# Performance work log

Hardware: AMD Instinct MI355X
Metric: run time of the kernel (lower is better)

The kernel has to match this reference:

```python
import jax, jax.numpy as jnp
import numpy as np

N_NODES = 100000
N_EDGES = 600000
D_FEAT = 128
D_DOT = 4


def setup_inputs() -> dict:
    key = jax.random.key(0)
    k1, k2, k3, k4, k5 = jax.random.split(key, 5)
    n = jax.random.normal(k1, (N_NODES, D_FEAT), dtype=jnp.float32)
    e = jax.random.normal(k2, (N_EDGES, D_FEAT), dtype=jnp.float32)
    # xavier_uniform for Linear(D_FEAT, D_DOT); bias filled with 0
    limit = float(np.sqrt(6.0 / (D_FEAT + D_DOT)))
    W = jax.random.uniform(k3, (D_DOT, D_FEAT), dtype=jnp.float32, minval=-limit, maxval=limit)
    b = jnp.zeros((D_DOT,), dtype=jnp.float32)
    src_idx = jax.random.randint(k4, (N_EDGES,), 0, N_NODES, dtype=jnp.int64)
    dst_idx = jax.random.randint(k5, (N_EDGES,), 0, N_NODES, dtype=jnp.int64)
    return {"n": n, "e": e, "W": W, "b": b, "src_idx": src_idx, "dst_idx": dst_idx}


def reference(n, e, W, b, src_idx, dst_idx):
    # gather per-edge src/dst node features: [E, D]
    src = n[src_idx]
    dst = n[dst_idx]
    # include_edge_features=True: mean of node and edge features
    src = (src + e) * 0.5
    dst = (dst + e) * 0.5
    # tiny linear projection to dot_product_dim=4: [E, 4]
    hs = src @ W.T + b
    hd = dst @ W.T + b
    # per-edge dot product (bmm of [E,1,4] x [E,4,1] -> [E,1]) then sigmoid
    score = jax.nn.sigmoid(jnp.sum(hs * hd, axis=-1, keepdims=True))
    return score
```

## Files before the change

### kernel.cpp

```cpp
#include <hip/hip_runtime.h>
#include <math.h>

#define D_FEAT 128
#define D_DOT  4


__device__ __forceinline__ float dot4(const float4 a, const float4 b) {
    return a.x * b.x + a.y * b.y + a.z * b.z + a.w * b.w;
}

__global__ __launch_bounds__(256, 6) void node_proj_kernel(
    const float* __restrict__ n,
    const float* __restrict__ W,
    float* __restrict__ pn,
    int n_nodes)
{
    const int t    = threadIdx.x;
    const int lane = t & 63;
    const int sub  = lane & 15;
    const int g    = lane >> 4;
    const int wave = t >> 6;
    const int base = blockIdx.x * 32 + wave * 8;
    const int last = n_nodes - 1;

    const float4* W4 = reinterpret_cast<const float4*>(W);
    float4 wlo[D_DOT], whi[D_DOT];
#pragma unroll
    for (int k = 0; k < D_DOT; ++k) {
        wlo[k] = W4[k * 32 + sub];
        whi[k] = W4[k * 32 + sub + 16];
    }

    const int rA = base + g;
    const int rB = base + 4 + g;
    const int cA = rA > last ? last : rA;
    const int cB = rB > last ? last : rB;
    const float4* pA = reinterpret_cast<const float4*>(n) + (size_t)cA * 32;
    const float4* pB = reinterpret_cast<const float4*>(n) + (size_t)cB * 32;
    const float4 xAl = pA[sub], xAh = pA[sub + 16];
    const float4 xBl = pB[sub], xBh = pB[sub + 16];

    float a[D_DOT], c[D_DOT];
#pragma unroll
    for (int k = 0; k < D_DOT; ++k) {
        a[k] = dot4(xAl, wlo[k]) + dot4(xAh, whi[k]);
        c[k] = dot4(xBl, wlo[k]) + dot4(xBh, whi[k]);
    }
#pragma unroll
    for (int m = 8; m >= 1; m >>= 1) {
#pragma unroll
        for (int k = 0; k < D_DOT; ++k) {
            a[k] += __shfl_xor(a[k], m, 64);
            c[k] += __shfl_xor(c[k], m, 64);
        }
    }
    if (sub == 0 && rA < n_nodes)
        reinterpret_cast<float4*>(pn)[rA] = make_float4(a[0], a[1], a[2], a[3]);
    if (sub == 0 && rB < n_nodes)
        reinterpret_cast<float4*>(pn)[rB] = make_float4(c[0], c[1], c[2], c[3]);
}

__global__ __launch_bounds__(256, 6) void edge_score_kernel(
    const float* __restrict__ e,
    const float* __restrict__ W,
    const float* __restrict__ bias,
    const float* __restrict__ pn,
    const int* __restrict__ src_idx,
    const int* __restrict__ dst_idx,
    float* __restrict__ out,
    int n_edges)
{
    const int t    = threadIdx.x;
    const int lane = t & 63;
    const int sub  = lane & 15;
    const int g    = lane >> 4;
    const int wave = t >> 6;
    const int base = blockIdx.x * 32 + wave * 8;
    const int last = n_edges - 1;

    const float4* W4 = reinterpret_cast<const float4*>(W);
    float4 wlo[D_DOT], whi[D_DOT];
#pragma unroll
    for (int k = 0; k < D_DOT; ++k) {
        wlo[k] = W4[k * 32 + sub];
        whi[k] = W4[k * 32 + sub + 16];
    }
    const float b0 = bias[0], b1 = bias[1], b2 = bias[2], b3 = bias[3];

    const int rA = base + g;
    const int rB = base + 4 + g;
    const int cA = rA > last ? last : rA;
    const int cB = rB > last ? last : rB;
    const float4* pAp = reinterpret_cast<const float4*>(e) + (size_t)cA * 32;
    const float4* pBp = reinterpret_cast<const float4*>(e) + (size_t)cB * 32;
    const float4 xAl = pAp[sub], xAh = pAp[sub + 16];
    const float4 xBl = pBp[sub], xBh = pBp[sub + 16];

    float a[D_DOT], c[D_DOT];
#pragma unroll
    for (int k = 0; k < D_DOT; ++k) {
        a[k] = dot4(xAl, wlo[k]) + dot4(xAh, whi[k]);
        c[k] = dot4(xBl, wlo[k]) + dot4(xBh, whi[k]);
    }
#pragma unroll
    for (int m = 8; m >= 1; m >>= 1) {
#pragma unroll
        for (int k = 0; k < D_DOT; ++k) {
            a[k] += __shfl_xor(a[k], m, 64);
            c[k] += __shfl_xor(c[k], m, 64);
        }
    }

    if (sub == 0 && rA < n_edges) {
        const int s = src_idx[rA];
        const int d = dst_idx[rA];
        const float4 ps = reinterpret_cast<const float4*>(pn)[s];
        const float4 pd = reinterpret_cast<const float4*>(pn)[d];
        const float u0 = 0.5f * a[0] + b0, u1 = 0.5f * a[1] + b1;
        const float u2 = 0.5f * a[2] + b2, u3 = 0.5f * a[3] + b3;
        float dot = (0.5f * ps.x + u0) * (0.5f * pd.x + u0)
                  + (0.5f * ps.y + u1) * (0.5f * pd.y + u1)
                  + (0.5f * ps.z + u2) * (0.5f * pd.z + u2)
                  + (0.5f * ps.w + u3) * (0.5f * pd.w + u3);
        out[rA] = 1.0f / (1.0f + __expf(-dot));
    }
    if (sub == 0 && rB < n_edges) {
        const int s = src_idx[rB];
        const int d = dst_idx[rB];
        const float4 ps = reinterpret_cast<const float4*>(pn)[s];
        const float4 pd = reinterpret_cast<const float4*>(pn)[d];
        const float u0 = 0.5f * c[0] + b0, u1 = 0.5f * c[1] + b1;
        const float u2 = 0.5f * c[2] + b2, u3 = 0.5f * c[3] + b3;
        float dot = (0.5f * ps.x + u0) * (0.5f * pd.x + u0)
                  + (0.5f * ps.y + u1) * (0.5f * pd.y + u1)
                  + (0.5f * ps.z + u2) * (0.5f * pd.z + u2)
                  + (0.5f * ps.w + u3) * (0.5f * pd.w + u3);
        out[rB] = 1.0f / (1.0f + __expf(-dot));
    }
}

extern "C" void kernel_launch(void* const* d_in, const int* in_sizes, int n_in,
                              void* d_out, int out_size, void* d_ws, size_t ws_size,
                              hipStream_t stream) {
    const float* n    = (const float*)d_in[0];
    const float* e    = (const float*)d_in[1];
    const float* W    = (const float*)d_in[2];
    const float* bias = (const float*)d_in[3];
    const int*   src  = (const int*)d_in[4];
    const int*   dst  = (const int*)d_in[5];
    float* out = (float*)d_out;

    const int n_nodes = in_sizes[0] / D_FEAT;
    const int n_edges = in_sizes[1] / D_FEAT;

    float* pn = (float*)d_ws;

    const int nblk = (n_nodes + 31) / 32;
    const int eblk = (n_edges + 31) / 32;
    node_proj_kernel<<<nblk, 256, 0, stream>>>(n, W, pn, n_nodes);
    edge_score_kernel<<<eblk, 256, 0, stream>>>(e, W, bias, pn, src, dst, out, n_edges);
}
```

Measured before the change: 82.53 us.

## Hoist index and projected-node gathers before reduction; use DPP row reductions

The edge kernel now loads src/dst indices and the projected node vectors at the start, clamped to valid rows, so those dependent gathers overlap with the edge-feature loads instead of following the reduction. Both kernels replace the xor-shuffle butterfly with DPP row_shr adds that leave the 16-lane sum in the last lane of each row. Launch bounds drop to 4 waves per SIMD, and feature loads are issued before the weight loads. One risk: with row_shr the full sum lands in lane 15 of each row, not lane 0, but lane 0 (sub==0) is still the lane that stores, so the stored values may be wrong.

```diff
diff --git a/kernel.cpp b/kernel.cpp
--- a/kernel.cpp
+++ b/kernel.cpp
@@ -9,7 +9,23 @@
     return a.x * b.x + a.y * b.y + a.z * b.z + a.w * b.w;
 }
 
-__global__ __launch_bounds__(256, 6) void node_proj_kernel(
+template <int CTRL>
+__device__ __forceinline__ float dpp_add(float x) {
+    union { float f; int i; } u, v;
+    u.f = x;
+    v.i = __builtin_amdgcn_update_dpp(u.i, u.i, CTRL, 0xF, 0xF, true);
+    return x + v.f;
+}
+
+__device__ __forceinline__ float row_reduce16(float x) {
+    x = dpp_add<0x128>(x);
+    x = dpp_add<0x124>(x);
+    x = dpp_add<0x122>(x);
+    x = dpp_add<0x121>(x);
+    return x;
+}
+
+__global__ __launch_bounds__(256, 4) void node_proj_kernel(
     const float* __restrict__ n,
     const float* __restrict__ W,
     float* __restrict__ pn,
@@ -23,6 +39,15 @@
     const int base = blockIdx.x * 32 + wave * 8;
     const int last = n_nodes - 1;
 
+    const int rA = base + g;
+    const int rB = base + 4 + g;
+    const int cA = rA > last ? last : rA;
+    const int cB = rB > last ? last : rB;
+
+    const float4* n4 = reinterpret_cast<const float4*>(n);
+    const float4 xAl = n4[(size_t)cA * 32 + sub], xAh = n4[(size_t)cA * 32 + sub + 16];
+    const float4 xBl = n4[(size_t)cB * 32 + sub], xBh = n4[(size_t)cB * 32 + sub + 16];
+
     const float4* W4 = reinterpret_cast<const float4*>(W);
     float4 wlo[D_DOT], whi[D_DOT];
 #pragma unroll
@@ -31,15 +56,6 @@
         whi[k] = W4[k * 32 + sub + 16];
     }
 
-    const int rA = base + g;
-    const int rB = base + 4 + g;
-    const int cA = rA > last ? last : rA;
-    const int cB = rB > last ? last : rB;
-    const float4* pA = reinterpret_cast<const float4*>(n) + (size_t)cA * 32;
-    const float4* pB = reinterpret_cast<const float4*>(n) + (size_t)cB * 32;
-    const float4 xAl = pA[sub], xAh = pA[sub + 16];
-    const float4 xBl = pB[sub], xBh = pB[sub + 16];
-
     float a[D_DOT], c[D_DOT];
 #pragma unroll
     for (int k = 0; k < D_DOT; ++k) {
@@ -47,20 +63,18 @@
         c[k] = dot4(xBl, wlo[k]) + dot4(xBh, whi[k]);
     }
 #pragma unroll
-    for (int m = 8; m >= 1; m >>= 1) {
-#pragma unroll
-        for (int k = 0; k < D_DOT; ++k) {
-            a[k] += __shfl_xor(a[k], m, 64);
-            c[k] += __shfl_xor(c[k], m, 64);
-        }
+    for (int k = 0; k < D_DOT; ++k) {
+        a[k] = row_reduce16(a[k]);
+        c[k] = row_reduce16(c[k]);
     }
+
     if (sub == 0 && rA < n_nodes)
         reinterpret_cast<float4*>(pn)[rA] = make_float4(a[0], a[1], a[2], a[3]);
     if (sub == 0 && rB < n_nodes)
         reinterpret_cast<float4*>(pn)[rB] = make_float4(c[0], c[1], c[2], c[3]);
 }
 
-__global__ __launch_bounds__(256, 6) void edge_score_kernel(
+__global__ __launch_bounds__(256, 4) void edge_score_kernel(
     const float* __restrict__ e,
     const float* __restrict__ W,
     const float* __restrict__ bias,
@@ -78,6 +92,22 @@
     const int base = blockIdx.x * 32 + wave * 8;
     const int last = n_edges - 1;
 
+    const int rA = base + g;
+    const int rB = base + 4 + g;
+    const int cA = rA > last ? last : rA;
+    const int cB = rB > last ? last : rB;
+
+    const int sA = src_idx[cA], dA = dst_idx[cA];
+    const int sB = src_idx[cB], dB = dst_idx[cB];
+
+    const float4* pn4 = reinterpret_cast<const float4*>(pn);
+    const float4 psA = pn4[sA], pdA = pn4[dA];
+    const float4 psB = pn4[sB], pdB = pn4[dB];
+
+    const float4* e4 = reinterpret_cast<const float4*>(e);
+    const float4 xAl = e4[(size_t)cA * 32 + sub], xAh = e4[(size_t)cA * 32 + sub + 16];
+    const float4 xBl = e4[(size_t)cB * 32 + sub], xBh = e4[(size_t)cB * 32 + sub + 16];
+
     const float4* W4 = reinterpret_cast<const float4*>(W);
     float4 wlo[D_DOT], whi[D_DOT];
 #pragma unroll
@@ -87,15 +117,6 @@
     }
     const float b0 = bias[0], b1 = bias[1], b2 = bias[2], b3 = bias[3];
 
-    const int rA = base + g;
-    const int rB = base + 4 + g;
-    const int cA = rA > last ? last : rA;
-    const int cB = rB > last ? last : rB;
-    const float4* pAp = reinterpret_cast<const float4*>(e) + (size_t)cA * 32;
-    const float4* pBp = reinterpret_cast<const float4*>(e) + (size_t)cB * 32;
-    const float4 xAl = pAp[sub], xAh = pAp[sub + 16];
-    const float4 xBl = pBp[sub], xBh = pBp[sub + 16];
-
     float a[D_DOT], c[D_DOT];
 #pragma unroll
     for (int k = 0; k < D_DOT; ++k) {
@@ -103,39 +124,30 @@
         c[k] = dot4(xBl, wlo[k]) + dot4(xBh, whi[k]);
     }
 #pragma unroll
-    for (int m = 8; m >= 1; m >>= 1) {
-#pragma unroll
-        for (int k = 0; k < D_DOT; ++k) {
-            a[k] += __shfl_xor(a[k], m, 64);
-            c[k] += __shfl_xor(c[k], m, 64);
-        }
+    for (int k = 0; k < D_DOT; ++k) {
+        a[k] = row_reduce16(a[k]);
+        c[k] = row_reduce16(c[k]);
     }
 
-    if (sub == 0 && rA < n_edges) {
-        const int s = src_idx[rA];
-        const int d = dst_idx[rA];
-        const float4 ps = reinterpret_cast<const float4*>(pn)[s];
-        const float4 pd = reinterpret_cast<const float4*>(pn)[d];
+    {
         const float u0 = 0.5f * a[0] + b0, u1 = 0.5f * a[1] + b1;
         const float u2 = 0.5f * a[2] + b2, u3 = 0.5f * a[3] + b3;
-        float dot = (0.5f * ps.x + u0) * (0.5f * pd.x + u0)
-                  + (0.5f * ps.y + u1) * (0.5f * pd.y + u1)
-                  + (0.5f * ps.z + u2) * (0.5f * pd.z + u2)
-                  + (0.5f * ps.w + u3) * (0.5f * pd.w + u3);
-        out[rA] = 1.0f / (1.0f + __expf(-dot));
+        const float dot = (0.5f * psA.x + u0) * (0.5f * pdA.x + u0)
+                        + (0.5f * psA.y + u1) * (0.5f * pdA.y + u1)
+                        + (0.5f * psA.z + u2) * (0.5f * pdA.z + u2)
+                        + (0.5f * psA.w + u3) * (0.5f * pdA.w + u3);
+        if (sub == 0 && rA < n_edges)
+            out[rA] = 1.0f / (1.0f + __expf(-dot));
     }
-    if (sub == 0 && rB < n_edges) {
-        const int s = src_idx[rB];
-        const int d = dst_idx[rB];
-        const float4 ps = reinterpret_cast<const float4*>(pn)[s];
-        const float4 pd = reinterpret_cast<const float4*>(pn)[d];
+    {
         const float u0 = 0.5f * c[0] + b0, u1 = 0.5f * c[1] + b1;
         const float u2 = 0.5f * c[2] + b2, u3 = 0.5f * c[3] + b3;
-        float dot = (0.5f * ps.x + u0) * (0.5f * pd.x + u0)
-                  + (0.5f * ps.y + u1) * (0.5f * pd.y + u1)
-                  + (0.5f * ps.z + u2) * (0.5f * pd.z + u2)
-                  + (0.5f * ps.w + u3) * (0.5f * pd.w + u3);
-        out[rB] = 1.0f / (1.0f + __expf(-dot));
+        const float dot = (0.5f * psB.x + u0) * (0.5f * pdB.x + u0)
+                        + (0.5f * psB.y + u1) * (0.5f * pdB.y + u1)
+                        + (0.5f * psB.z + u2) * (0.5f * pdB.z + u2)
+                        + (0.5f * psB.w + u3) * (0.5f * pdB.w + u3);
+        if (sub == 0 && rB < n_edges)
+            out[rB] = 1.0f / (1.0f + __expf(-dot));
     }
 }
 
```

After: 80.84 us. -2.0%, faster.
